# Kernel optimization log

Hardware: AMD Instinct MI355X
Metric: run time of the kernel (lower is better)

Reference implementation:

```python
import jax, jax.numpy as jnp
import numpy as np

THR = 1.0     # snntorch Leaky default threshold
BETA = 0.9    # args.beta
ALPHA = 2.0   # surrogate.atan default alpha

@jax.custom_vjp
def atan_spike(x):
    # Heaviside forward, arctan surrogate gradient (snntorch surrogate.atan)
    return (x > 0).astype(x.dtype)

def _aspk_fwd(x):
    return atan_spike(x), x

def _aspk_bwd(x, g):
    return (g * (ALPHA / 2.0) / (1.0 + (jnp.pi / 2.0 * ALPHA * x) ** 2),)

atan_spike.defvjp(_aspk_fwd, _aspk_bwd)

def setup_inputs() -> dict:
    key = jax.random.key(0)
    k = jax.random.split(key, 5)
    B, D, H, C = 32768, 187, 50, 5
    return {
        "x": jax.random.normal(k[0], (B, D), dtype=jnp.float32),
        "W1": jax.random.normal(k[1], (H, D), dtype=jnp.float32) * (1.0 / np.sqrt(D)),
        "b1": jax.random.normal(k[2], (H,), dtype=jnp.float32) * 0.01,
        "W2": jax.random.normal(k[3], (C, H), dtype=jnp.float32) * (1.0 / np.sqrt(H)),
        "b2": jax.random.normal(k[4], (C,), dtype=jnp.float32) * 0.01,
        "num_steps": 100,
    }

def reference(x, W1, b1, W2, b2, num_steps):
    B = x.shape[0]
    dt = x.dtype
    # fc1(x) is identical every timestep (x is static), compute once
    cur1 = x @ W1.T + b1  # [B, 50]

    def step(carry, _):
        mem1, mem2 = carry
        # Leaky: reset computed from PREVIOUS mem (detached), subtract mechanism
        reset1 = jax.lax.stop_gradient((mem1 > THR).astype(dt))
        mem1 = BETA * mem1 + cur1 - reset1 * THR
        spk1 = atan_spike(mem1 - THR)
        cur2 = spk1 @ W2.T + b2  # [B, num_classes]
        reset2 = jax.lax.stop_gradient((mem2 > THR).astype(dt))
        mem2 = BETA * mem2 + cur2 - reset2 * THR
        spk2 = atan_spike(mem2 - THR)
        return (mem1, mem2), (spk2, mem2)

    init = (jnp.zeros((B, W1.shape[0]), dt), jnp.zeros((B, W2.shape[0]), dt))
    _, (spk_rec, mem_rec) = jax.lax.scan(step, init, None, length=num_steps)
    return spk_rec, mem_rec  # each [num_steps, B, num_classes]
```

## Files before the change

kernel.cpp:

```cpp
#include <hip/hip_runtime.h>

typedef float v2f __attribute__((ext_vector_type(2)));

#define DD   187
#define HH   50
#define PH   56
#define HPJ  14
#define NP   7
#define NC   5
#define RPB  64
#define BLK  256
#define DCH  64
#define NCHUNK 3
#define BETA 0.9f

__device__ __forceinline__ float dpp_xor1(float v) {
    return __builtin_bit_cast(float,
        __builtin_amdgcn_mov_dpp(__builtin_bit_cast(int, v), 0xB1, 0xF, 0xF, true));
}
__device__ __forceinline__ float dpp_xor2(float v) {
    return __builtin_bit_cast(float,
        __builtin_amdgcn_mov_dpp(__builtin_bit_cast(int, v), 0x4E, 0xF, 0xF, true));
}

__device__ __forceinline__ float spike1(float m) {
    float t = fmaf(m, 0x1.0p60f, -0x1.0p60f);
    return fminf(fmaxf(t, 0.f), 1.f);
}
__device__ __forceinline__ v2f spike2(v2f m) {
    const v2f BIG2  = { 0x1.0p60f,  0x1.0p60f};
    const v2f NBIG2 = {-0x1.0p60f, -0x1.0p60f};
    const v2f ONE2  = {1.f, 1.f};
    const v2f ZERO2 = {0.f, 0.f};
    v2f t = __builtin_elementwise_fma(m, BIG2, NBIG2);
    return __builtin_elementwise_min(__builtin_elementwise_max(t, ZERO2), ONE2);
}

__global__ __launch_bounds__(BLK, 2)
void snn_kernel(const float* __restrict__ x,
                const float* __restrict__ W1,
                const float* __restrict__ b1,
                const float* __restrict__ W2,
                const float* __restrict__ b2,
                const int*   __restrict__ nsp,
                float* __restrict__ out, int Brows)
{
    __shared__ float xs[RPB * 65];
    __shared__ float w1t[DCH * PH];

    const int tid = threadIdx.x;
    const int p   = tid >> 2;
    const int k   = tid & 3;
    const int row = blockIdx.x * RPB + p;
    const int NS  = nsp[0];

    v2f acc[NP];
#pragma unroll
    for (int i = 0; i < NP; ++i) acc[i] = (v2f){0.f, 0.f};

    for (int ch = 0; ch < NCHUNK; ++ch) {
        const int d0 = ch * DCH;
        for (int i = tid; i < RPB * DCH; i += BLK) {
            int r = i >> 6, dd = i & 63;
            int d = d0 + dd;
            xs[r * 65 + dd] = (d < DD) ? x[(size_t)(blockIdx.x * RPB + r) * DD + d] : 0.f;
        }
        for (int i = tid; i < DCH * PH; i += BLK) {
            int h = i >> 6, dd = i & 63;
            int d = d0 + dd;
            w1t[dd * PH + h] = (h < HH && d < DD) ? W1[h * DD + d] : 0.f;
        }
        __syncthreads();

        const float* xr = xs + p * 65;
#pragma unroll 4
        for (int d = 0; d < DCH; ++d) {
            float xv = xr[d];
            const v2f* wr = (const v2f*)(w1t + d * PH + k * HPJ);
            v2f xvv = {xv, xv};
#pragma unroll
            for (int i = 0; i < NP; ++i)
                acc[i] = __builtin_elementwise_fma(xvv, wr[i], acc[i]);
        }
        __syncthreads();
    }

    v2f c1[NP];
#pragma unroll
    for (int i = 0; i < NP; ++i) {
        int h0 = k * HPJ + 2 * i;
        v2f bb = { (h0     < HH) ? b1[h0]     : 0.f,
                   (h0 + 1 < HH) ? b1[h0 + 1] : 0.f };
        c1[i] = acc[i] + bb;
    }

    v2f w2r[NC][NP];
#pragma unroll
    for (int c = 0; c < NC; ++c)
#pragma unroll
        for (int i = 0; i < NP; ++i) {
            int h0 = k * HPJ + 2 * i;
            w2r[c][i] = { (h0     < HH) ? W2[c * HH + h0]     : 0.f,
                          (h0 + 1 < HH) ? W2[c * HH + h0 + 1] : 0.f };
        }
    const float b2A = b2[k];
    const float b2B = b2[4];

    v2f m1[NP], s1[NP];
#pragma unroll
    for (int i = 0; i < NP; ++i) { m1[i] = (v2f){0.f, 0.f}; s1[i] = (v2f){0.f, 0.f}; }
    float mA = 0.f, sA = 0.f, mB = 0.f, sB = 0.f;

    const size_t stride = (size_t)Brows * NC;
    float* spkBase = out;
    float* memBase = out + (size_t)NS * stride;
    const int offA = row * NC + k;
    const int offB = row * NC + 4;
    const v2f BETA2 = {BETA, BETA};

    for (int t = 0; t < NS; ++t) {
        v2f cp[NC];
#pragma unroll
        for (int c = 0; c < NC; ++c) cp[c] = (v2f){0.f, 0.f};
#pragma unroll
        for (int i = 0; i < NP; ++i) {
            v2f m = __builtin_elementwise_fma(BETA2, m1[i], c1[i]) - s1[i];
            m1[i] = m;
            v2f s = spike2(m);
            s1[i] = s;
#pragma unroll
            for (int c = 0; c < NC; ++c)
                cp[c] = __builtin_elementwise_fma(s, w2r[c][i], cp[c]);
        }
        float cur2[NC];
#pragma unroll
        for (int c = 0; c < NC; ++c) {
            float r = cp[c].x + cp[c].y;
            r += dpp_xor1(r);
            r += dpp_xor2(r);
            cur2[c] = r;
        }
        float cA = (k == 0) ? cur2[0] : (k == 1) ? cur2[1] : (k == 2) ? cur2[2] : cur2[3];
        float cB = cur2[4];

        mA = fmaf(BETA, mA, cA + b2A) - sA;
        sA = spike1(mA);
        mB = fmaf(BETA, mB, cB + b2B) - sB;
        sB = spike1(mB);

        spkBase[offA] = sA;
        memBase[offA] = mA;
        if (k == 0) { spkBase[offB] = sB; memBase[offB] = mB; }

        spkBase += stride;
        memBase += stride;
    }
}

extern "C" void kernel_launch(void* const* d_in, const int* in_sizes, int n_in,
                              void* d_out, int out_size, void* d_ws, size_t ws_size,
                              hipStream_t stream) {
    const float* x  = (const float*)d_in[0];
    const float* W1 = (const float*)d_in[1];
    const float* b1 = (const float*)d_in[2];
    const float* W2 = (const float*)d_in[3];
    const float* b2 = (const float*)d_in[4];
    const int*   ns = (const int*)d_in[5];
    int B = in_sizes[0] / DD;
    int nblocks = B / RPB;
    snn_kernel<<<nblocks, BLK, 0, stream>>>(x, W1, b1, W2, b2, ns, (float*)d_out, B);
}
```

Measured before the change: 217.7 us.

## Split each row across eight lanes and fold the output bias into the hidden weights

```diff
diff --git a/kernel.cpp b/kernel.cpp
--- a/kernel.cpp
+++ b/kernel.cpp
@@ -1,17 +1,19 @@
 #include <hip/hip_runtime.h>
 
 typedef float v2f __attribute__((ext_vector_type(2)));
+typedef float v4f __attribute__((ext_vector_type(4)));
 
 #define DD   187
 #define HH   50
-#define PH   56
-#define HPJ  14
-#define NP   7
+#define PH   64
+#define HPJ  8
+#define NP   4
 #define NC   5
-#define RPB  64
+#define RPB  32
 #define BLK  256
 #define DCH  64
 #define NCHUNK 3
+#define XSS  68
 #define BETA 0.9f
 
 __device__ __forceinline__ float dpp_xor1(float v) {
@@ -21,6 +23,10 @@
 __device__ __forceinline__ float dpp_xor2(float v) {
     return __builtin_bit_cast(float,
         __builtin_amdgcn_mov_dpp(__builtin_bit_cast(int, v), 0x4E, 0xF, 0xF, true));
+}
+__device__ __forceinline__ float dpp_xor8(float v) {
+    return __builtin_bit_cast(float,
+        __builtin_amdgcn_mov_dpp(__builtin_bit_cast(int, v), 0x128, 0xF, 0xF, true));
 }
 
 __device__ __forceinline__ float spike1(float m) {
@@ -36,7 +42,7 @@
     return __builtin_elementwise_min(__builtin_elementwise_max(t, ZERO2), ONE2);
 }
 
-__global__ __launch_bounds__(BLK, 2)
+__global__ __launch_bounds__(BLK, 4)
 void snn_kernel(const float* __restrict__ x,
                 const float* __restrict__ W1,
                 const float* __restrict__ b1,
@@ -45,12 +51,15 @@
                 const int*   __restrict__ nsp,
                 float* __restrict__ out, int Brows)
 {
-    __shared__ float xs[RPB * 65];
+    __shared__ float xs[RPB * XSS];
     __shared__ float w1t[DCH * PH];
 
     const int tid = threadIdx.x;
-    const int p   = tid >> 2;
-    const int k   = tid & 3;
+    const int l   = tid & 15;
+    const int g   = tid >> 4;
+    const int hb  = (l >> 2) & 1;
+    const int p   = g * 2 + hb;
+    const int k   = (l & 3) | ((l & 8) >> 1);
     const int row = blockIdx.x * RPB + p;
     const int NS  = nsp[0];
 
@@ -63,24 +72,31 @@
         for (int i = tid; i < RPB * DCH; i += BLK) {
             int r = i >> 6, dd = i & 63;
             int d = d0 + dd;
-            xs[r * 65 + dd] = (d < DD) ? x[(size_t)(blockIdx.x * RPB + r) * DD + d] : 0.f;
+            xs[r * XSS + dd] = (d < DD) ? x[(size_t)(blockIdx.x * RPB + r) * DD + d] : 0.f;
         }
         for (int i = tid; i < DCH * PH; i += BLK) {
-            int h = i >> 6, dd = i & 63;
+            int dd = i >> 6, h = i & 63;
             int d = d0 + dd;
             w1t[dd * PH + h] = (h < HH && d < DD) ? W1[h * DD + d] : 0.f;
         }
         __syncthreads();
 
-        const float* xr = xs + p * 65;
+        const float* xr = xs + p * XSS;
 #pragma unroll 4
-        for (int d = 0; d < DCH; ++d) {
-            float xv = xr[d];
-            const v2f* wr = (const v2f*)(w1t + d * PH + k * HPJ);
-            v2f xvv = {xv, xv};
+        for (int d4 = 0; d4 < DCH / 4; ++d4) {
+            v4f xv4 = *(const v4f*)(xr + 4 * d4);
 #pragma unroll
-            for (int i = 0; i < NP; ++i)
-                acc[i] = __builtin_elementwise_fma(xvv, wr[i], acc[i]);
+            for (int j = 0; j < 4; ++j) {
+                int d = 4 * d4 + j;
+                const v4f* wr = (const v4f*)(w1t + d * PH + k * HPJ);
+                v4f wa = wr[0], wb = wr[1];
+                float xv = xv4[j];
+                v2f xvv = {xv, xv};
+                acc[0] = __builtin_elementwise_fma(xvv, __builtin_shufflevector(wa, wa, 0, 1), acc[0]);
+                acc[1] = __builtin_elementwise_fma(xvv, __builtin_shufflevector(wa, wa, 2, 3), acc[1]);
+                acc[2] = __builtin_elementwise_fma(xvv, __builtin_shufflevector(wb, wb, 0, 1), acc[2]);
+                acc[3] = __builtin_elementwise_fma(xvv, __builtin_shufflevector(wb, wb, 2, 3), acc[3]);
+            }
         }
         __syncthreads();
     }
@@ -89,10 +105,12 @@
 #pragma unroll
     for (int i = 0; i < NP; ++i) {
         int h0 = k * HPJ + 2 * i;
-        v2f bb = { (h0     < HH) ? b1[h0]     : 0.f,
-                   (h0 + 1 < HH) ? b1[h0 + 1] : 0.f };
+        v2f bb;
+        bb.x = (h0     < HH) ? b1[h0]     : 0.f;
+        bb.y = (h0 + 1 < HH) ? b1[h0 + 1] : 0.f;
         c1[i] = acc[i] + bb;
     }
+    if (k == 7) c1[3].y = 2.0f;
 
     v2f w2r[NC][NP];
 #pragma unroll
@@ -100,22 +118,24 @@
 #pragma unroll
         for (int i = 0; i < NP; ++i) {
             int h0 = k * HPJ + 2 * i;
-            w2r[c][i] = { (h0     < HH) ? W2[c * HH + h0]     : 0.f,
-                          (h0 + 1 < HH) ? W2[c * HH + h0 + 1] : 0.f };
+            w2r[c][i].x = (h0     < HH) ? W2[c * HH + h0]     : 0.f;
+            w2r[c][i].y = (h0 + 1 < HH) ? W2[c * HH + h0 + 1] : 0.f;
         }
-    const float b2A = b2[k];
-    const float b2B = b2[4];
+    if (k == 7) {
+#pragma unroll
+        for (int c = 0; c < NC; ++c) w2r[c][3].y = b2[c];
+    }
 
     v2f m1[NP], s1[NP];
 #pragma unroll
     for (int i = 0; i < NP; ++i) { m1[i] = (v2f){0.f, 0.f}; s1[i] = (v2f){0.f, 0.f}; }
-    float mA = 0.f, sA = 0.f, mB = 0.f, sB = 0.f;
+    float mA = 0.f, sA = 0.f;
 
     const size_t stride = (size_t)Brows * NC;
     float* spkBase = out;
     float* memBase = out + (size_t)NS * stride;
     const int offA = row * NC + k;
-    const int offB = row * NC + 4;
+    const bool owner = (k < NC);
     const v2f BETA2 = {BETA, BETA};
 
     for (int t = 0; t < NS; ++t) {
@@ -138,20 +158,19 @@
             float r = cp[c].x + cp[c].y;
             r += dpp_xor1(r);
             r += dpp_xor2(r);
+            r += dpp_xor8(r);
             cur2[c] = r;
         }
-        float cA = (k == 0) ? cur2[0] : (k == 1) ? cur2[1] : (k == 2) ? cur2[2] : cur2[3];
-        float cB = cur2[4];
+        float cA = (k == 1) ? cur2[1] : (k == 2) ? cur2[2] :
+                   (k == 3) ? cur2[3] : (k == 4) ? cur2[4] : cur2[0];
 
-        mA = fmaf(BETA, mA, cA + b2A) - sA;
+        mA = fmaf(BETA, mA, cA) - sA;
         sA = spike1(mA);
-        mB = fmaf(BETA, mB, cB + b2B) - sB;
-        sB = spike1(mB);
 
-        spkBase[offA] = sA;
-        memBase[offA] = mA;
-        if (k == 0) { spkBase[offB] = sB; memBase[offB] = mB; }
-
+        if (owner) {
+            spkBase[offA] = sA;
+            memBase[offA] = mA;
+        }
         spkBase += stride;
         memBase += stride;
     }
```

Result: slower. 232.4 us (+6.8%).
